# Optimization experiments

Hardware: AMD Instinct MI355X
Metric: run time of the kernel (lower is better)

Reference implementation:

```python
import jax, jax.numpy as jnp
import numpy as np

B, C_IN, T, H, W = 32, 1024, 7, 14, 14
C_INTER = 512


def setup_inputs() -> dict:
    key = jax.random.key(0)
    ks = jax.random.split(key, 8)
    s = lambda fan_in: 1.0 / np.sqrt(fan_in)
    return {
        "x_window": jax.random.normal(ks[0], (B, C_IN, T, H, W), jnp.float32),
        "nodes": jax.random.normal(ks[1], (T, C_INTER), jnp.float32),
        "Wq": jax.random.normal(ks[2], (C_IN, C_INTER), jnp.float32) * s(C_IN),
        "bq": jnp.zeros((C_INTER,), jnp.float32),
        "Wk": jax.random.normal(ks[3], (C_INTER, C_INTER), jnp.float32) * s(C_INTER),
        "bk": jnp.zeros((C_INTER,), jnp.float32),
        "Wv": jax.random.normal(ks[4], (C_IN, C_INTER), jnp.float32) * s(C_IN),
        "bv": jnp.zeros((C_INTER,), jnp.float32),
        "Wo": jax.random.normal(ks[5], (C_INTER, C_IN), jnp.float32) * s(C_INTER),
        "bo": jnp.zeros((C_IN,), jnp.float32),
    }


def reference(x_window, nodes, Wq, bq, Wk, bk, Wv, bv, Wo, bo):
    # x_window: (B, C_in, T, H, W); dropout is identity at eval time.
    t_mid = x_window.shape[2] // 2
    x_item = x_window[:, :, t_mid]                                   # (B, C_in, H, W)
    # pointwise (Linear3d) projections over channel dim
    query = jnp.einsum("bchw,cd->bdhw", x_item, Wq) + bq[None, :, None, None]
    key = nodes @ Wk + bk                                            # (T, C_inter)
    value = jnp.einsum("bcthw,cd->bdthw", x_window, Wv) + bv[None, :, None, None, None]
    # per-pixel attention scores over the T node keys
    alpha = jnp.einsum("bdhw,td->bthw", query, key)                  # (B, T, H, W)
    alpha = jax.nn.softmax(alpha, axis=1)
    # per-pixel weighted temporal sum
    y = jnp.einsum("bthw,bdthw->bdhw", alpha, value)                 # (B, C_inter, H, W)
    out = jnp.einsum("bdhw,dc->bchw", y, Wo) + bo[None, :, None, None]
    return out[:, :, None]                                           # (B, C_in, 1, H, W)
```

## Files before the change

kernel.cpp:

```cpp
#include <hip/hip_runtime.h>
#include <hip/hip_bf16.h>
#include <hip/hip_cooperative_groups.h>
#include <stdint.h>

namespace cg = cooperative_groups;

#define BB    32
#define CIN   1024
#define TT    7
#define HHWW  196
#define HW4   49
#define CI    512
#define TMID  3
#define MM    (BB*HHWW)
#define NCH   16
#define CSZ   64
#define GRID  512

using bf16 = __hip_bfloat16;
typedef __attribute__((ext_vector_type(8))) short short8;
typedef __attribute__((ext_vector_type(4))) short s16x4;
typedef __attribute__((ext_vector_type(4))) float f32x4;

__device__ __forceinline__ void gload_lds16(const void* g, void* l) {
    __builtin_amdgcn_global_load_lds((const __attribute__((address_space(1))) void*)g,
                                     (__attribute__((address_space(3))) void*)l, 16, 0, 0);
}

__device__ __forceinline__ void ctr_inc(int* p) {
    __hip_atomic_fetch_add(p, 1, __ATOMIC_RELEASE, __HIP_MEMORY_SCOPE_AGENT);
}
__device__ __forceinline__ int ctr_inc_acqrel(int* p) {
    return __hip_atomic_fetch_add(p, 1, __ATOMIC_ACQ_REL, __HIP_MEMORY_SCOPE_AGENT);
}
__device__ __forceinline__ void ctr_wait(int* p, int tgt) {
    while (__hip_atomic_load(p, __ATOMIC_ACQUIRE, __HIP_MEMORY_SCOPE_AGENT) < tgt)
        __builtin_amdgcn_s_sleep(8);
}

template <int EPI>
__device__ __forceinline__ void gemm_body(const bf16* __restrict__ A, const bf16* __restrict__ Bt,
                                          void* __restrict__ Cout, const float* __restrict__ bias,
                                          int M, int N, int K, int bm, int bn,
                                          bf16* As, bf16* Bs) {
    int tid = threadIdx.x;
    int wid = tid >> 6, lane = tid & 63;
    int wr = wid >> 1, wc = wid & 1;
    f32x4 acc[4][4] = {};
    const bf16* Ab = A + (size_t)bm * 128 * K;
    const bf16* Bb = Bt + (size_t)bn * 128 * K;
    int row = lane & 15;
    int kb_base = (lane >> 4) * 8;

    for (int k0 = 0; k0 < K; k0 += 64) {
        #pragma unroll
        for (int it = 0; it < 4; ++it) {
            int e = (it * 256 + tid) * 8;
            int r = e >> 6, cc = e & 63;
            gload_lds16(Ab + (size_t)r * K + k0 + cc, &As[e]);
            gload_lds16(Bb + (size_t)r * K + k0 + cc, &Bs[e]);
        }
        __syncthreads();
        #pragma unroll
        for (int kk = 0; kk < 2; ++kk) {
            int kb = kk * 32 + kb_base;
            short8 a[4], b[4];
            #pragma unroll
            for (int mi = 0; mi < 4; ++mi) a[mi] = *(const short8*)&As[(wr * 64 + mi * 16 + row) * 64 + kb];
            #pragma unroll
            for (int ni = 0; ni < 4; ++ni) b[ni] = *(const short8*)&Bs[(wc * 64 + ni * 16 + row) * 64 + kb];
            #pragma unroll
            for (int mi = 0; mi < 4; ++mi)
                #pragma unroll
                for (int ni = 0; ni < 4; ++ni)
                    acc[mi][ni] = __builtin_amdgcn_mfma_f32_16x16x32_bf16(a[mi], b[ni], acc[mi][ni], 0, 0, 0);
        }
        __syncthreads();
    }

    int col_l = lane & 15, row_l = (lane >> 4) * 4;
    if constexpr (EPI == 0) {
        bf16* C = (bf16*)Cout;
        #pragma unroll
        for (int mi = 0; mi < 4; ++mi) {
            int row0 = bm * 128 + wr * 64 + mi * 16 + row_l;
            #pragma unroll
            for (int ni = 0; ni < 4; ++ni) {
                int col = bn * 128 + wc * 64 + ni * 16 + col_l;
                #pragma unroll
                for (int r = 0; r < 4; ++r)
                    C[(size_t)(row0 + r) * N + col] = __float2bfloat16(acc[mi][ni][r]);
            }
        }
    } else {
        float* Cf = (float*)Cout;
        #pragma unroll
        for (int ni = 0; ni < 4; ++ni) {
            int n = bn * 128 + wc * 64 + ni * 16 + col_l;
            float bz = bias[n];
            #pragma unroll
            for (int mi = 0; mi < 4; ++mi) {
                int m0 = bm * 128 + wr * 64 + mi * 16 + row_l;
                int b = m0 / HHWW;
                int hw0 = m0 - b * HHWW;
                f32x4 v = acc[mi][ni];
                v[0] += bz; v[1] += bz; v[2] += bz; v[3] += bz;
                *(f32x4*)&Cf[((size_t)b * CIN + n) * HHWW + hw0] = v;
            }
        }
    }
}

__device__ __forceinline__ void phase_prep1_unit(
    int u, int tid, float* sred,
    const float* __restrict__ nodes, const float* __restrict__ Wk, const float* __restrict__ bk,
    float* __restrict__ key,
    const float* __restrict__ Wv, const float* __restrict__ Wo,
    bf16* __restrict__ Wv_bf, bf16* __restrict__ WoT_bf,
    const float* __restrict__ bv, const float* __restrict__ bo, float* __restrict__ bvo) {
    if (u < 56) {
        int t = u >> 3, dc = u & 7;
        int d_l = tid & 63, q = tid >> 6;
        int d = dc * 64 + d_l;
        float acc = 0.f;
        const float* nr = nodes + t * CI;
        #pragma unroll 4
        for (int c = q * 128; c < q * 128 + 128; ++c)
            acc = fmaf(nr[c], Wk[(size_t)c * CI + d], acc);
        sred[q * 64 + d_l] = acc;
        __syncthreads();
        if (q == 0)
            key[t * CI + d] = sred[d_l] + sred[64 + d_l] + sred[128 + d_l] + sred[192 + d_l] + bk[d];
    } else if (u < 56 + 2048) {
        int i = (u - 56) * 256 + tid;
        Wv_bf[i] = __float2bfloat16(Wv[i]);
        int d = i >> 10, cp = i & 1023;
        WoT_bf[(size_t)cp * CI + d] = __float2bfloat16(Wo[i]);
    } else {
        int cp0 = (u - 2104) * 32;
        int cp_l = tid & 31, dq = tid >> 5;
        float acc = 0.f;
        #pragma unroll 4
        for (int d = dq * 64; d < dq * 64 + 64; ++d)
            acc = fmaf(bv[d], Wo[(size_t)d * CIN + cp0 + cp_l], acc);
        sred[dq * 32 + cp_l] = acc;
        __syncthreads();
        if (dq == 0) {
            float v = bo[cp0 + cp_l];
            #pragma unroll
            for (int g = 0; g < 8; ++g) v += sred[g * 32 + cp_l];
            bvo[cp0 + cp_l] = v;
        }
    }
}

__device__ __forceinline__ void phase_wqk_unit(
    int cbase, int tid,
    const float* __restrict__ Wq, const float* __restrict__ bq,
    const float* __restrict__ key, float* __restrict__ Wqk, float* __restrict__ bqk) {
    int c = cbase + (tid >> 6);
    int lane = tid & 63;
    if (c > CIN) return;
    const float* src = (c < CIN) ? (Wq + (size_t)c * CI) : bq;
    float acc[TT] = {};
    #pragma unroll 2
    for (int it = 0; it < CI / 64; ++it) {
        float w = src[it * 64 + lane];
        #pragma unroll
        for (int t = 0; t < TT; ++t) acc[t] = fmaf(w, key[t * CI + it * 64 + lane], acc[t]);
    }
    #pragma unroll
    for (int t = 0; t < TT; ++t) {
        float v = acc[t];
        for (int off = 32; off; off >>= 1) v += __shfl_down(v, off);
        if (lane == 0) { if (c < CIN) Wqk[c * 8 + t] = v; else bqk[t] = v; }
    }
}

__device__ __forceinline__ void phase_alpha_unit(
    int ch, int b, int tid, float* wq_s,
    const float* __restrict__ x, const float* __restrict__ Wqk, float* __restrict__ part) {
    for (int i = tid; i < CSZ * 8; i += 256) wq_s[i] = Wqk[ch * CSZ * 8 + i];
    __syncthreads();
    if (tid < HHWW) {
        float acc[TT] = {};
        const float* xb = x + (size_t)(b * CIN + ch * CSZ) * TT * HHWW + TMID * HHWW + tid;
        #pragma unroll 8
        for (int c = 0; c < CSZ; ++c) {
            float v = xb[(size_t)c * TT * HHWW];
            #pragma unroll
            for (int t = 0; t < TT; ++t) acc[t] = fmaf(v, wq_s[c * 8 + t], acc[t]);
        }
        #pragma unroll
        for (int t = 0; t < TT; ++t)
            part[((size_t)(b * NCH + ch) * TT + t) * HHWW + tid] = acc[t];
    }
}

__device__ __forceinline__ void phase_softmax_unit(
    int b, int tid,
    const float* __restrict__ part, const float* __restrict__ bqk, float* __restrict__ alphaF) {
    if (tid >= HHWW) return;
    float s[TT];
    #pragma unroll
    for (int t = 0; t < TT; ++t) s[t] = bqk[t];
    for (int ch = 0; ch < NCH; ++ch)
        #pragma unroll
        for (int t = 0; t < TT; ++t)
            s[t] += part[((size_t)(b * NCH + ch) * TT + t) * HHWW + tid];
    float mx = s[0];
    #pragma unroll
    for (int t = 1; t < TT; ++t) mx = fmaxf(mx, s[t]);
    float e[TT], sum = 0.f;
    #pragma unroll
    for (int t = 0; t < TT; ++t) { e[t] = __expf(s[t] - mx); sum += e[t]; }
    float inv = 1.f / sum;
    #pragma unroll
    for (int t = 0; t < TT; ++t) alphaF[(size_t)b * TT * HHWW + t * HHWW + tid] = e[t] * inv;
}

__device__ __forceinline__ void phase_smxw_unit(
    int c0, int b, int tid, float* al, bf16* txp,
    const float* __restrict__ x, const float* __restrict__ alphaF, bf16* __restrict__ xw) {
    for (int i = tid; i < TT * HHWW; i += 256) al[i] = alphaF[(size_t)b * TT * HHWW + i];
    __syncthreads();
    const f32x4* xp = (const f32x4*)x;
    f32x4 acc[7] = {};
    #pragma unroll
    for (int t = 0; t < TT; ++t) {
        #pragma unroll
        for (int k = 0; k < 7; ++k) {
            int w = k * 256 + tid;
            if (k == 6 && w >= 1568) continue;
            int c_l = w / 49;
            int hw4 = w - c_l * 49;
            f32x4 a4 = *(const f32x4*)&al[t * HHWW + hw4 * 4];
            f32x4 xv = xp[((size_t)(b * CIN + c0 + c_l) * TT + t) * HW4 + hw4];
            acc[k] += a4 * xv;
        }
    }
    #pragma unroll
    for (int k = 0; k < 7; ++k) {
        int w = k * 256 + tid;
        if (k == 6 && w >= 1568) continue;
        int c_l = w / 49;
        int hw4 = w - c_l * 49;
        int v = (hw4 & 7) << 2;
        #pragma unroll
        for (int r = 0; r < 4; ++r)
            txp[(hw4 * 4 + r) * 32 + (c_l ^ v)] = __float2bfloat16(acc[k][r]);
    }
    __syncthreads();
    #pragma unroll
    for (int k = 0; k < 7; ++k) {
        int w = k * 256 + tid;
        if (k == 6 && w >= 1568) continue;
        int m = w >> 3, seg = w & 7;
        int v = ((m >> 2) & 7) << 2;
        s16x4 val = *(const s16x4*)&txp[m * 32 + ((seg * 4) ^ v)];
        *(s16x4*)&xw[(size_t)(b * HHWW + m) * CIN + c0 + seg * 4] = val;
    }
}

__global__ __launch_bounds__(256, 2) void mega(
    const float* __restrict__ x, const float* __restrict__ nodes,
    const float* __restrict__ Wq, const float* __restrict__ bq,
    const float* __restrict__ Wk, const float* __restrict__ bk,
    const float* __restrict__ Wv, const float* __restrict__ bv,
    const float* __restrict__ Wo, const float* __restrict__ bo,
    float* __restrict__ key, float* __restrict__ Wqk, float* __restrict__ bqk,
    float* __restrict__ bvo, bf16* __restrict__ Wv_bf, bf16* __restrict__ WoT_bf,
    bf16* __restrict__ WvoT, float* __restrict__ part, float* __restrict__ alphaF,
    bf16* __restrict__ xw, float* __restrict__ out, int* ctr) {

    cg::grid_group grid = cg::this_grid();
    __shared__ __align__(16) char smem[32768];
    __shared__ int sflag;
    bf16* As = (bf16*)smem;
    bf16* Bs = (bf16*)(smem + 16384);
    int gid = blockIdx.x, tid = threadIdx.x;

    if (gid == 0 && tid < 128) ctr[tid] = 0;
    for (int u = gid; u < 2136; u += GRID) {
        __syncthreads();
        phase_prep1_unit(u, tid, (float*)smem, nodes, Wk, bk, key, Wv, Wo, Wv_bf, WoT_bf, bv, bo, bvo);
    }
    grid.sync();

    if (gid < 257) {
        phase_wqk_unit(gid * 4, tid, Wq, bq, key, Wqk, bqk);
        __syncthreads();
        if (tid == 0) { __threadfence(); ctr_inc(&ctr[97]); }
    } else if (gid >= 448) {
        int t0 = gid - 448;
        gemm_body<0>(WoT_bf, Wv_bf, (void*)WvoT, nullptr, 1024, 1024, 512, t0 >> 3, t0 & 7, As, Bs);
        __syncthreads();
        if (tid == 0) { __threadfence(); ctr_inc(&ctr[96]); }
    }

    if (gid < 448) {
        if (tid == 0) ctr_wait(&ctr[97], 257);
        __syncthreads();
        int nu = (gid < 64) ? 2 : 1;
        for (int r = 0; r < nu; ++r) {
            int u = (r == 0) ? gid : (448 + gid);
            int b = u >> 4, ch = u & 15;
            __syncthreads();
            phase_alpha_unit(ch, b, tid, (float*)smem, x, Wqk, part);
            __syncthreads();
            if (tid == 0) sflag = (ctr_inc_acqrel(&ctr[b]) == NCH - 1);
            __syncthreads();
            if (sflag) {
                phase_softmax_unit(b, tid, part, bqk, alphaF);
                __syncthreads();
                if (tid == 0) { __threadfence(); ctr_inc(&ctr[32 + b]); }
            }
        }
    }

    #pragma unroll 1
    for (int r = 0; r < 2; ++r) {
        int u = gid + r * GRID;
        int b = u >> 5, c0 = (u & 31) * 32;
        if (tid == 0) ctr_wait(&ctr[32 + b], 1);
        __syncthreads();
        phase_smxw_unit(c0, b, tid, (float*)smem, (bf16*)(smem + 5504), x, alphaF, xw);
        __syncthreads();
        if (tid == 0) { __threadfence(); ctr_inc(&ctr[64 + b]); }
    }

    if (gid < 392) {
        int bm = gid >> 3, bn = gid & 7;
        int b0 = (bm * 128) / HHWW, b1 = (bm * 128 + 127) / HHWW;
        if (tid == 0) {
            ctr_wait(&ctr[96], 64);
            ctr_wait(&ctr[64 + b0], 32);
            ctr_wait(&ctr[64 + b1], 32);
        }
        __syncthreads();
        gemm_body<1>(xw, WvoT, (void*)out, bvo, MM, CIN, CIN, bm, bn, As, Bs);
    }
}

__global__ __launch_bounds__(256) void k_prep1(
    const float* __restrict__ nodes, const float* __restrict__ Wk, const float* __restrict__ bk,
    float* __restrict__ key, const float* __restrict__ Wv, const float* __restrict__ Wo,
    bf16* __restrict__ Wv_bf, bf16* __restrict__ WoT_bf,
    const float* __restrict__ bv, const float* __restrict__ bo, float* __restrict__ bvo) {
    __shared__ float sred[256];
    phase_prep1_unit(blockIdx.x, threadIdx.x, sred, nodes, Wk, bk, key, Wv, Wo, Wv_bf, WoT_bf, bv, bo, bvo);
}

__global__ __launch_bounds__(256) void k_prep2(
    const bf16* __restrict__ WoT_bf, const bf16* __restrict__ Wv_bf, bf16* __restrict__ WvoT,
    const float* __restrict__ Wq, const float* __restrict__ bq,
    const float* __restrict__ key, float* __restrict__ Wqk, float* __restrict__ bqk) {
    __shared__ __align__(16) bf16 As[128 * 64];
    __shared__ __align__(16) bf16 Bs[128 * 64];
    int bid = blockIdx.x;
    if (bid < 64) gemm_body<0>(WoT_bf, Wv_bf, (void*)WvoT, nullptr, 1024, 1024, 512, bid >> 3, bid & 7, As, Bs);
    else phase_wqk_unit((bid - 64) * 4, threadIdx.x, Wq, bq, key, Wqk, bqk);
}

__global__ __launch_bounds__(256) void k_alpha(const float* __restrict__ x,
                                               const float* __restrict__ Wqk,
                                               float* __restrict__ part) {
    __shared__ float wq_s[CSZ * 8];
    phase_alpha_unit(blockIdx.x, blockIdx.y, threadIdx.x, wq_s, x, Wqk, part);
}

__global__ __launch_bounds__(256) void k_softmaxF(const float* __restrict__ part,
                                                  const float* __restrict__ bqk,
                                                  float* __restrict__ alphaF) {
    phase_softmax_unit(blockIdx.x, threadIdx.x, part, bqk, alphaF);
}

__global__ __launch_bounds__(256) void k_smxw(const float* __restrict__ x,
                                              const float* __restrict__ alphaF,
                                              bf16* __restrict__ xw) {
    __shared__ __align__(16) float al[TT * HHWW];
    __shared__ __align__(16) bf16 txp[HHWW * 32];
    phase_smxw_unit(blockIdx.x * 32, blockIdx.y, threadIdx.x, al, txp, x, alphaF, xw);
}

__global__ __launch_bounds__(256) void k_gemm1(const bf16* __restrict__ A, const bf16* __restrict__ Bt,
                                               float* __restrict__ C, const float* __restrict__ bias) {
    __shared__ __align__(16) bf16 As[128 * 64];
    __shared__ __align__(16) bf16 Bs[128 * 64];
    gemm_body<1>(A, Bt, (void*)C, bias, MM, CIN, CIN, blockIdx.x, blockIdx.y, As, Bs);
}

extern "C" void kernel_launch(void* const* d_in, const int* in_sizes, int n_in,
                              void* d_out, int out_size, void* d_ws, size_t ws_size,
                              hipStream_t stream) {
    const float* x     = (const float*)d_in[0];
    const float* nodes = (const float*)d_in[1];
    const float* Wq    = (const float*)d_in[2];
    const float* bq    = (const float*)d_in[3];
    const float* Wk    = (const float*)d_in[4];
    const float* bk    = (const float*)d_in[5];
    const float* Wv    = (const float*)d_in[6];
    const float* bv    = (const float*)d_in[7];
    const float* Wo    = (const float*)d_in[8];
    const float* bo    = (const float*)d_in[9];

    uint8_t* w = (uint8_t*)d_ws;
    size_t off = 0;
    auto alloc = [&](size_t bytes) -> void* {
        void* p = w + off;
        off = (off + bytes + 255) & ~(size_t)255;
        return p;
    };
    float* key    = (float*)alloc((size_t)TT * CI * 4);
    float* Wqk    = (float*)alloc((size_t)CIN * 8 * 4);
    float* bqk    = (float*)alloc(8 * 4);
    float* bvo    = (float*)alloc((size_t)CIN * 4);
    bf16*  Wv_bf  = (bf16*)alloc((size_t)CIN * CI * 2);
    bf16*  WoT_bf = (bf16*)alloc((size_t)CIN * CI * 2);
    bf16*  WvoT   = (bf16*)alloc((size_t)CIN * CIN * 2);
    float* part   = (float*)alloc((size_t)BB * NCH * TT * HHWW * 4);
    float* alphaF = (float*)alloc((size_t)BB * TT * HHWW * 4);
    bf16*  xw     = (bf16*)alloc((size_t)MM * CIN * 2);
    int*   ctr    = (int*)alloc(128 * 4);
    float* outp   = (float*)d_out;
    (void)ws_size;

    bool use_coop = false;
    int dev = 0;
    if (hipGetDevice(&dev) == hipSuccess) {
        int coop = 0, ncu = 0, nb = 0;
        hipDeviceGetAttribute(&coop, hipDeviceAttributeCooperativeLaunch, dev);
        hipDeviceGetAttribute(&ncu, hipDeviceAttributeMultiprocessorCount, dev);
        if (coop == 1 &&
            hipOccupancyMaxActiveBlocksPerMultiprocessor(&nb, (const void*)mega, 256, 0) == hipSuccess &&
            nb * ncu >= GRID) {
            use_coop = true;
        }
    }

    if (use_coop) {
        void* kargs[] = {
            (void*)&x, (void*)&nodes, (void*)&Wq, (void*)&bq, (void*)&Wk, (void*)&bk,
            (void*)&Wv, (void*)&bv, (void*)&Wo, (void*)&bo,
            (void*)&key, (void*)&Wqk, (void*)&bqk, (void*)&bvo,
            (void*)&Wv_bf, (void*)&WoT_bf, (void*)&WvoT, (void*)&part, (void*)&alphaF,
            (void*)&xw, (void*)&outp, (void*)&ctr
        };
        if (hipLaunchCooperativeKernel((const void*)mega, dim3(GRID), dim3(256), kargs, 0, stream)
            == hipSuccess)
            return;
    }

    k_prep1<<<2136, 256, 0, stream>>>(nodes, Wk, bk, key, Wv, Wo, Wv_bf, WoT_bf, bv, bo, bvo);
    k_prep2<<<321, 256, 0, stream>>>(WoT_bf, Wv_bf, WvoT, Wq, bq, key, Wqk, bqk);
    k_alpha<<<dim3(NCH, BB), 256, 0, stream>>>(x, Wqk, part);
    k_softmaxF<<<BB, 256, 0, stream>>>(part, bqk, alphaF);
    k_smxw<<<dim3(32, BB), 256, 0, stream>>>(x, alphaF, xw);
    k_gemm1<<<dim3(49, 8), 256, 0, stream>>>(xw, WvoT, (float*)d_out, bvo);
}
```

Measured before the change: 102.0 us.

## Replace static phase assignment with atomic work queue interleaving smxw and GEMM tiles

The fixed per-block phases after the grid sync (alpha, smxw, output GEMM) become a dynamic work queue. Each block pulls items from an atomic counter. Smxw units and output-GEMM tiles are interleaved in groups so GEMM tiles can start as soon as their batches' xw rows are ready, overlapping the stages and balancing load across blocks. The cost is one atomic fetch plus two extra barriers per item, and a risk of spin-wait stalls if queue order puts dependents ahead of their producers.

```diff
diff --git a/kernel.cpp b/kernel.cpp
--- a/kernel.cpp
+++ b/kernel.cpp
@@ -16,6 +16,7 @@
 #define NCH   16
 #define CSZ   64
 #define GRID  512
+#define QTOT  1928
 
 using bf16 = __hip_bfloat16;
 typedef __attribute__((ext_vector_type(8))) short short8;
@@ -32,6 +33,9 @@
 }
 __device__ __forceinline__ int ctr_inc_acqrel(int* p) {
     return __hip_atomic_fetch_add(p, 1, __ATOMIC_ACQ_REL, __HIP_MEMORY_SCOPE_AGENT);
+}
+__device__ __forceinline__ int ctr_next(int* p) {
+    return __hip_atomic_fetch_add(p, 1, __ATOMIC_RELAXED, __HIP_MEMORY_SCOPE_AGENT);
 }
 __device__ __forceinline__ void ctr_wait(int* p, int tgt) {
     while (__hip_atomic_load(p, __ATOMIC_ACQUIRE, __HIP_MEMORY_SCOPE_AGENT) < tgt)
@@ -275,7 +279,7 @@
 
     cg::grid_group grid = cg::this_grid();
     __shared__ __align__(16) char smem[32768];
-    __shared__ int sflag;
+    __shared__ int sitem, sflag;
     bf16* As = (bf16*)smem;
     bf16* Bs = (bf16*)(smem + 16384);
     int gid = blockIdx.x, tid = threadIdx.x;
@@ -298,13 +302,16 @@
         if (tid == 0) { __threadfence(); ctr_inc(&ctr[96]); }
     }
 
-    if (gid < 448) {
-        if (tid == 0) ctr_wait(&ctr[97], 257);
-        __syncthreads();
-        int nu = (gid < 64) ? 2 : 1;
-        for (int r = 0; r < nu; ++r) {
-            int u = (r == 0) ? gid : (448 + gid);
-            int b = u >> 4, ch = u & 15;
+    while (true) {
+        __syncthreads();
+        if (tid == 0) sitem = ctr_next(&ctr[98]);
+        __syncthreads();
+        int i = sitem;
+        if (i >= QTOT) break;
+
+        if (i < 512) {
+            int b = i >> 4, ch = i & 15;
+            if (tid == 0) ctr_wait(&ctr[97], 257);
             __syncthreads();
             phase_alpha_unit(ch, b, tid, (float*)smem, x, Wqk, part);
             __syncthreads();
@@ -315,30 +322,35 @@
                 __syncthreads();
                 if (tid == 0) { __threadfence(); ctr_inc(&ctr[32 + b]); }
             }
-        }
-    }
-
-    #pragma unroll 1
-    for (int r = 0; r < 2; ++r) {
-        int u = gid + r * GRID;
-        int b = u >> 5, c0 = (u & 31) * 32;
-        if (tid == 0) ctr_wait(&ctr[32 + b], 1);
-        __syncthreads();
-        phase_smxw_unit(c0, b, tid, (float*)smem, (bf16*)(smem + 5504), x, alphaF, xw);
-        __syncthreads();
-        if (tid == 0) { __threadfence(); ctr_inc(&ctr[64 + b]); }
-    }
-
-    if (gid < 392) {
-        int bm = gid >> 3, bn = gid & 7;
-        int b0 = (bm * 128) / HHWW, b1 = (bm * 128 + 127) / HHWW;
-        if (tid == 0) {
-            ctr_wait(&ctr[96], 64);
-            ctr_wait(&ctr[64 + b0], 32);
-            ctr_wait(&ctr[64 + b1], 32);
-        }
-        __syncthreads();
-        gemm_body<1>(xw, WvoT, (void*)out, bvo, MM, CIN, CIN, bm, bn, As, Bs);
+        } else {
+            int j = i - 512;
+            int su = -1, t = -1;
+            if (j < 64) su = j;
+            else if (j < 1384) {
+                int gg = (j - 64) / 44, r = (j - 64) % 44;
+                if (r < 32) su = 64 + gg * 32 + r;
+                else        t = gg * 12 + (r - 32);
+            } else t = 360 + (j - 1384);
+
+            if (su >= 0) {
+                int b = su >> 5, c0 = (su & 31) * 32;
+                if (tid == 0) ctr_wait(&ctr[32 + b], 1);
+                __syncthreads();
+                phase_smxw_unit(c0, b, tid, (float*)smem, (bf16*)(smem + 5504), x, alphaF, xw);
+                __syncthreads();
+                if (tid == 0) { __threadfence(); ctr_inc(&ctr[64 + b]); }
+            } else {
+                int bm = t >> 3, bn = t & 7;
+                int b0 = (bm * 128) / HHWW, b1 = (bm * 128 + 127) / HHWW;
+                if (tid == 0) {
+                    ctr_wait(&ctr[96], 64);
+                    ctr_wait(&ctr[64 + b0], 32);
+                    ctr_wait(&ctr[64 + b1], 32);
+                }
+                __syncthreads();
+                gemm_body<1>(xw, WvoT, (void*)out, bvo, MM, CIN, CIN, bm, bn, As, Bs);
+            }
+        }
     }
 }
 
```

New measurement: 102.4 us. Within noise of the previous version (+0.3%).
